# Performance work log

Hardware: AMD Instinct MI355X
Metric: run time of the kernel (lower is better)

## Reference

```python
import jax, jax.numpy as jnp
import numpy as np

B, D, K = 32768, 256, 2048
BETA = 0.25


def setup_inputs() -> dict:
    key = jax.random.key(0)
    k1, k2 = jax.random.split(key)
    latents = jax.random.normal(k1, (B, D), dtype=jnp.float32)
    # nn.Embedding weight initialized uniform(-1/K, 1/K)
    embedding = jax.random.uniform(k2, (K, D), dtype=jnp.float32,
                                   minval=-1.0 / K, maxval=1.0 / K)
    return {"latents": latents, "embedding": embedding}


def reference(latents, embedding):
    # Squared-L2 distances: [B, K]
    dist = (jnp.sum(latents ** 2, axis=1, keepdims=True)
            + jnp.sum(embedding ** 2, axis=1)
            - 2.0 * jnp.matmul(latents, embedding.T))
    encoding_inds = jnp.argmin(dist, axis=1)  # [B]

    # Gather codebook rows (equivalent to one-hot @ embedding)
    quantized = embedding[encoding_inds]  # [B, D]

    commitment_loss = jnp.mean((jax.lax.stop_gradient(quantized) - latents) ** 2)
    embedding_loss = jnp.mean((quantized - jax.lax.stop_gradient(latents)) ** 2)
    vq_loss = commitment_loss * BETA + embedding_loss

    # Straight-through estimator
    quantized_st = latents + jax.lax.stop_gradient(quantized - latents)

    # avg_probs = mean of one-hot over batch == normalized histogram of inds
    counts = jnp.zeros((K,), dtype=jnp.float32).at[encoding_inds].add(1.0)
    avg_probs = counts / B
    entropy_vq = -jnp.sum(avg_probs * jnp.log(avg_probs + 1e-10))

    # dist values at selected codes
    cluster_metric = jnp.mean(
        jnp.take_along_axis(dist, encoding_inds[:, None], axis=1))

    return (quantized_st, vq_loss, entropy_vq,
            encoding_inds[:, None], cluster_metric)
```

## Files before the change

### kernel.cpp

```cpp
#include <hip/hip_runtime.h>
#include <math.h>

#define B_ROWS 32768
#define D_DIM  256
#define K_CODES 2048

#define OUT_Q   0
#define OUT_VQ  8388608
#define OUT_ENT 8388609
#define OUT_IND 8388610
#define OUT_CM  8421378


#define WS_SE2   0
#define WS_SX2   8192
#define WS_CNT   139264
#define WS_PACK  147456
#define WS_MSEP  409600
#define WS_DISTP 475136
#define WS_BCAT  540672

typedef _Float16 f16x8 __attribute__((ext_vector_type(8)));
typedef float f32x4 __attribute__((ext_vector_type(4)));
typedef union { _Float16 h[4]; uint2 u2; } h4pack;

__global__ __launch_bounds__(256) void k_init(
    const float* __restrict__ X, const float* __restrict__ E,
    _Float16* __restrict__ A, _Float16* __restrict__ Bc,
    float* __restrict__ sx2, float* __restrict__ se2,
    unsigned long long* __restrict__ packed, int* __restrict__ counts) {
  int w = threadIdx.x >> 6, lane = threadIdx.x & 63;
  if (blockIdx.x < 8192) {
    int row = blockIdx.x * 4 + w;
    float4 v = ((const float4*)(X + (size_t)row * D_DIM))[lane];
    float s = v.x * v.x + v.y * v.y + v.z * v.z + v.w * v.w;
#pragma unroll
    for (int off = 32; off > 0; off >>= 1) s += __shfl_xor(s, off, 64);
    if (lane == 0) { sx2[row] = s; packed[row] = ~0ull; }
    h4pack hi, lo;
    hi.h[0] = (_Float16)v.x; hi.h[1] = (_Float16)v.y;
    hi.h[2] = (_Float16)v.z; hi.h[3] = (_Float16)v.w;
    lo.h[0] = (_Float16)((v.x - (float)hi.h[0]) * 4096.0f);
    lo.h[1] = (_Float16)((v.y - (float)hi.h[1]) * 4096.0f);
    lo.h[2] = (_Float16)((v.z - (float)hi.h[2]) * 4096.0f);
    lo.h[3] = (_Float16)((v.w - (float)hi.h[3]) * 4096.0f);
    *(uint2*)&A[(size_t)row * 512 + 4 * lane] = hi.u2;
    *(uint2*)&A[(size_t)row * 512 + 256 + 4 * lane] = lo.u2;
  } else {
    int bb = blockIdx.x - 8192;
    int row = bb * 4 + w;
    if (threadIdx.x < 4) counts[bb * 4 + threadIdx.x] = 0;
    float4 v = ((const float4*)(E + (size_t)row * D_DIM))[lane];
    float s = v.x * v.x + v.y * v.y + v.z * v.z + v.w * v.w;
#pragma unroll
    for (int off = 32; off > 0; off >>= 1) s += __shfl_xor(s, off, 64);
    if (lane == 0) se2[row] = s;
    const float S = 4194304.0f;
    const float SH = 0.000244140625f;
    float e0 = v.x * S, e1 = v.y * S, e2 = v.z * S, e3 = v.w * S;
    h4pack b1, b2, b3;
    b1.h[0] = (_Float16)e0; b1.h[1] = (_Float16)e1;
    b1.h[2] = (_Float16)e2; b1.h[3] = (_Float16)e3;
    b2.h[0] = (_Float16)((float)b1.h[0] * SH);
    b2.h[1] = (_Float16)((float)b1.h[1] * SH);
    b2.h[2] = (_Float16)((float)b1.h[2] * SH);
    b2.h[3] = (_Float16)((float)b1.h[3] * SH);
    b3.h[0] = (_Float16)(e0 - (float)b1.h[0]);
    b3.h[1] = (_Float16)(e1 - (float)b1.h[1]);
    b3.h[2] = (_Float16)(e2 - (float)b1.h[2]);
    b3.h[3] = (_Float16)(e3 - (float)b1.h[3]);
    *(uint2*)&Bc[(size_t)row * 768 + 4 * lane] = b1.u2;
    *(uint2*)&Bc[(size_t)row * 768 + 256 + 4 * lane] = b2.u2;
    *(uint2*)&Bc[(size_t)row * 768 + 512 + 4 * lane] = b3.u2;
  }
}

#define BARX() asm volatile("s_barrier" ::: "memory")

#define MFMA_QUAD(I0, J0)                                                    \
  do {                                                                       \
    __builtin_amdgcn_s_setprio(1);                                           \
    _Pragma("unroll") for (int ii = 0; ii < 4; ++ii) {                       \
      _Pragma("unroll") for (int jj = 0; jj < 2; ++jj) {                     \
        _Pragma("unroll") for (int kk = 0; kk < 2; ++kk) {                   \
          acc[(I0) + ii][(J0) + jj] =                                        \
              __builtin_amdgcn_mfma_f32_16x16x32_f16(                        \
                  af[ii * 2 + kk], bf[jj * 2 + kk],                          \
                  acc[(I0) + ii][(J0) + jj], 0, 0, 0);                       \
        }                                                                    \
      }                                                                      \
    }                                                                        \
    __builtin_amdgcn_s_setprio(0);                                           \
  } while (0)

__global__ __launch_bounds__(512, 2) void k_mfma2(
    const _Float16* __restrict__ A, const _Float16* __restrict__ Bc,
    const float* __restrict__ se2, const float* __restrict__ sx2,
    unsigned long long* __restrict__ packed) {
  extern __shared__ char smem[];
  const int tid = threadIdx.x;
  const int w = tid >> 6, lane = tid & 63;
  const int wm = w >> 2, wn = w & 3;
  const int q = lane >> 4, c = lane & 15;
  const int rowb = blockIdx.x & 127, colb = blockIdx.x >> 7;
  const int rowpan = rowb * 256, colpan = colb * 256;
  const int rsel = lane >> 3;
  const int chunkb = ((lane & 7) ^ rsel) * 16;
  const int rswz = c & 7;

  const char* Abase = (const char*)A;
  const char* Bbase = (const char*)Bc;
  char* sA = smem;
  char* sB = smem + 65536;

  auto issue = [&](int tt, int g, int bsel) {
    const int hh = (g == 3 || g == 4 || g == 5 || g == 7) ? 1 : 0;
    const int ss = (g == 2 || g == 4 || g == 6 || g == 7) ? 1 : 0;
    const int rl = hh * 128 + ss * 64 + w * 8 + rsel;
    const char* src;
    char* dst;
    if (g == 0 || g >= 5) {
      int aoff = (tt & 3) * 128 + (((tt >> 2) == 1) ? 512 : 0);
      src = Abase + ((size_t)(rowpan + rl) << 10) + aoff + chunkb;
      dst = sA + bsel * 32768 + hh * 16384 + ss * 8192 + w * 1024;
    } else {
      src = Bbase + (size_t)(colpan + rl) * 1536 + tt * 128 + chunkb;
      dst = sB + bsel * 32768 + hh * 16384 + ss * 8192 + w * 1024;
    }
    __builtin_amdgcn_global_load_lds(
        (const __attribute__((address_space(1))) unsigned int*)src,
        (__attribute__((address_space(3))) unsigned int*)dst, 16, 0, 0);
  };

  f32x4 acc[8][4];
#pragma unroll
  for (int i = 0; i < 8; ++i)
#pragma unroll
    for (int j = 0; j < 4; ++j) acc[i][j] = (f32x4){0.f, 0.f, 0.f, 0.f};

  auto lda = [&](f16x8* af, int ihalf, int bsel) {
#pragma unroll
    for (int ii = 0; ii < 4; ++ii)
#pragma unroll
      for (int kk = 0; kk < 2; ++kk) {
        int row = wm * 128 + (ihalf * 4 + ii) * 16 + c;
        int sl = ((kk * 4 + q) ^ rswz) * 16;
        af[ii * 2 + kk] = *(const f16x8*)(sA + bsel * 32768 + row * 128 + sl);
      }
  };
  auto ldb = [&](f16x8* bf, int j0, int bsel) {
#pragma unroll
    for (int jj = 0; jj < 2; ++jj)
#pragma unroll
      for (int kk = 0; kk < 2; ++kk) {
        int col = wn * 64 + (j0 + jj) * 16 + c;
        int sl = ((kk * 4 + q) ^ rswz) * 16;
        bf[jj * 2 + kk] = *(const f16x8*)(sB + bsel * 32768 + col * 128 + sl);
      }
  };

#pragma unroll
  for (int g = 0; g < 8; ++g) issue(0, g, 0);
  asm volatile("s_waitcnt vmcnt(2)" ::: "memory");
  BARX();

  f16x8 af[8], bf[4];

  for (int t = 0; t < 12; ++t) {
    const int bsel = t & 1;
    const int nb = bsel ^ 1;
    const bool pre = (t < 11);
    lda(af, 0, bsel);
    ldb(bf, 0, bsel);
    if (pre) { issue(t + 1, 0, nb); issue(t + 1, 1, nb); }
    BARX();
    MFMA_QUAD(0, 0);
    BARX();
    ldb(bf, 2, bsel);
    if (pre) { issue(t + 1, 2, nb); issue(t + 1, 3, nb); }
    BARX();
    MFMA_QUAD(0, 2);
    if (pre) asm volatile("s_waitcnt vmcnt(4)" ::: "memory");
    else     asm volatile("s_waitcnt vmcnt(0)" ::: "memory");
    BARX();
    lda(af, 1, bsel);
    if (pre) { issue(t + 1, 4, nb); issue(t + 1, 5, nb); }
    BARX();
    MFMA_QUAD(4, 2);
    BARX();
    ldb(bf, 0, bsel);
    if (pre) { issue(t + 1, 6, nb); issue(t + 1, 7, nb); }
    BARX();
    MFMA_QUAD(4, 0);
    if (pre) asm volatile("s_waitcnt vmcnt(2)" ::: "memory");
    BARX();
  }

  const float inv = 4.76837158203125e-07f;
  float se_j[4];
#pragma unroll
  for (int j = 0; j < 4; ++j) se_j[j] = se2[colpan + wn * 64 + j * 16 + c];
  unsigned long long* m = (unsigned long long*)smem;
#pragma unroll
  for (int i = 0; i < 8; ++i) {
    float4 sx4 = *(const float4*)&sx2[rowpan + wm * 128 + i * 16 + q * 4];
#pragma unroll
    for (int r = 0; r < 4; ++r) {
      float sx = ((const float*)&sx4)[r];
      float bs = 3.402823466e38f;
      int bk = 0;
#pragma unroll
      for (int j = 0; j < 4; ++j) {
        float t1 = sx + se_j[j];
        float d = t1 - acc[i][j][r] * inv;
        if (d < bs) { bs = d; bk = colpan + wn * 64 + j * 16 + c; }
      }
#pragma unroll
      for (int off = 1; off < 16; off <<= 1) {
        float os = __shfl_xor(bs, off, 64);
        int ok = __shfl_xor(bk, off, 64);
        if (os < bs || (os == bs && ok < bk)) { bs = os; bk = ok; }
      }
      if (c == 0) {
        m[wn * 256 + wm * 128 + i * 16 + q * 4 + r] =
            ((unsigned long long)__float_as_uint(bs) << 32) |
            (unsigned long long)(unsigned int)bk;
      }
    }
  }
  __syncthreads();
  if (tid < 256) {
    unsigned long long v = m[tid];
#pragma unroll
    for (int mm = 1; mm < 4; ++mm) {
      unsigned long long o = m[mm * 256 + tid];
      if (o < v) v = o;
    }
    atomicMin(&packed[rowpan + tid], v);
  }
}

__global__ __launch_bounds__(256) void k_gather(
    const float* __restrict__ X, const float* __restrict__ E,
    const unsigned long long* __restrict__ packed, float* __restrict__ outq,
    float* __restrict__ out_ind, int* __restrict__ counts,
    double* __restrict__ msep, double* __restrict__ distp) {
  __shared__ int sk[16];
  __shared__ float sd[16];
  int tid = threadIdx.x;
  if (tid < 16) {
    int row = blockIdx.x * 16 + tid;
    unsigned long long v = packed[row];
    int k = (int)(v & 0xFFFFFFFFull);
    sk[tid] = k;
    sd[tid] = __uint_as_float((unsigned int)(v >> 32));
    out_ind[row] = (float)k;
    atomicAdd(&counts[k], 1);
  }
  __syncthreads();
  int wave = tid >> 6, lane = tid & 63;
  double msum = 0.0, dsum = 0.0;
#pragma unroll
  for (int rr = 0; rr < 4; rr++) {
    int li = wave * 4 + rr;
    int b = blockIdx.x * 16 + li;
    int ind = sk[li];
    float4 x4 = ((const float4*)(X + (size_t)b * D_DIM))[lane];
    float4 q4 = ((const float4*)(E + (size_t)ind * D_DIM))[lane];
    float d0 = q4.x - x4.x, d1 = q4.y - x4.y, d2 = q4.z - x4.z, d3 = q4.w - x4.w;
    float4 o;
    o.x = x4.x + d0; o.y = x4.y + d1; o.z = x4.z + d2; o.w = x4.w + d3;
    ((float4*)(outq + (size_t)b * D_DIM))[lane] = o;
    float v = d0 * d0 + d1 * d1 + d2 * d2 + d3 * d3;
#pragma unroll
    for (int off = 32; off > 0; off >>= 1) v += __shfl_xor(v, off, 64);
    if (lane == 0) { msum += (double)v; dsum += (double)sd[li]; }
  }
  if (lane == 0) {
    int wg = blockIdx.x * 4 + wave;
    msep[wg] = msum;
    distp[wg] = dsum;
  }
}

__global__ __launch_bounds__(256) void k_final(
    const int* __restrict__ counts, const double* __restrict__ msep,
    const double* __restrict__ distp, float* __restrict__ out) {
  __shared__ double red[256];
  int t = threadIdx.x;

  double m = 0.0;
  for (int i = t; i < 8192; i += 256) m += msep[i];
  red[t] = m;
  __syncthreads();
  for (int s = 128; s > 0; s >>= 1) {
    if (t < s) red[t] += red[t + s];
    __syncthreads();
  }
  if (t == 0) {
    double mse = red[0] / ((double)B_ROWS * (double)D_DIM);
    out[OUT_VQ] = (float)(mse * 1.25);
  }
  __syncthreads();

  double d = 0.0;
  for (int i = t; i < 8192; i += 256) d += distp[i];
  red[t] = d;
  __syncthreads();
  for (int s = 128; s > 0; s >>= 1) {
    if (t < s) red[t] += red[t + s];
    __syncthreads();
  }
  if (t == 0) out[OUT_CM] = (float)(red[0] / (double)B_ROWS);
  __syncthreads();

  double e = 0.0;
  for (int k = t; k < K_CODES; k += 256) {
    float p = (float)counts[k] * (1.0f / 32768.0f);
    e += (double)(p * logf(p + 1e-10f));
  }
  red[t] = e;
  __syncthreads();
  for (int s = 128; s > 0; s >>= 1) {
    if (t < s) red[t] += red[t + s];
    __syncthreads();
  }
  if (t == 0) out[OUT_ENT] = (float)(-red[0]);
}

extern "C" void kernel_launch(void* const* d_in, const int* in_sizes, int n_in,
                              void* d_out, int out_size, void* d_ws,
                              size_t ws_size, hipStream_t stream) {
  const float* X = (const float*)d_in[0];
  const float* E = (const float*)d_in[1];
  float* out = (float*)d_out;
  char* ws = (char*)d_ws;
  float* se2 = (float*)(ws + WS_SE2);
  float* sx2 = (float*)(ws + WS_SX2);
  int* counts = (int*)(ws + WS_CNT);
  unsigned long long* packed = (unsigned long long*)(ws + WS_PACK);
  double* msep = (double*)(ws + WS_MSEP);
  double* distp = (double*)(ws + WS_DISTP);
  _Float16* Bcat = (_Float16*)(ws + WS_BCAT);
  _Float16* Acat = (_Float16*)d_out;

  static bool attr_done = false;
  if (!attr_done) {
    hipFuncSetAttribute((const void*)k_mfma2,
                        hipFuncAttributeMaxDynamicSharedMemorySize, 131072);
    attr_done = true;
  }

  k_init<<<8704, 256, 0, stream>>>(X, E, Acat, Bcat, sx2, se2, packed, counts);
  k_mfma2<<<1024, 512, 131072, stream>>>(Acat, Bcat, se2, sx2, packed);
  k_gather<<<B_ROWS / 16, 256, 0, stream>>>(X, E, packed, out + OUT_Q,
                                            out + OUT_IND, counts, msep, distp);
  k_final<<<1, 256, 0, stream>>>(counts, msep, distp, out);
}
```

Measured before the change: 262.5 us.

## Hand-schedule LDS reads with inline ds_read and double B fragment registers

Replaces compiler-generated LDS fragment loads with inline ds_read_b128 using immediate offsets. B fragments for both column halves are now held in separate register sets (bf01, bf23), which removes one reload and one barrier phase per k-step. Explicit lgkmcnt waits and sched_barriers pin the instruction order so loads are issued before barriers and MFMAs run after them. This trades higher VGPR pressure, which risks the 2-waves-per-SIMD occupancy target, and more rigid scheduling for fewer LDS reads and barriers.

```diff
diff --git a/kernel.cpp b/kernel.cpp
--- a/kernel.cpp
+++ b/kernel.cpp
@@ -75,9 +75,17 @@
   }
 }
 
-#define BARX() asm volatile("s_barrier" ::: "memory")
-
-#define MFMA_QUAD(I0, J0)                                                    \
+#define BAR()  __builtin_amdgcn_s_barrier()
+#define SB0()  __builtin_amdgcn_sched_barrier(0)
+#define WLGKM0()                                                \
+  do {                                                          \
+    asm volatile("s_waitcnt lgkmcnt(0)" ::: "memory");          \
+    SB0();                                                      \
+  } while (0)
+#define DSR(dst, a, o) \
+  asm volatile("ds_read_b128 %0, %1 offset:" o : "=v"(dst) : "v"(a))
+
+#define MFMA_QUAD(I0, J0, BF)                                                \
   do {                                                                       \
     __builtin_amdgcn_s_setprio(1);                                           \
     _Pragma("unroll") for (int ii = 0; ii < 4; ++ii) {                       \
@@ -85,7 +93,7 @@
         _Pragma("unroll") for (int kk = 0; kk < 2; ++kk) {                   \
           acc[(I0) + ii][(J0) + jj] =                                        \
               __builtin_amdgcn_mfma_f32_16x16x32_f16(                        \
-                  af[ii * 2 + kk], bf[jj * 2 + kk],                          \
+                  af[ii * 2 + kk], (BF)[jj * 2 + kk],                        \
                   acc[(I0) + ii][(J0) + jj], 0, 0, 0);                       \
         }                                                                    \
       }                                                                      \
@@ -110,8 +118,6 @@
 
   const char* Abase = (const char*)A;
   const char* Bbase = (const char*)Bc;
-  char* sA = smem;
-  char* sB = smem + 65536;
 
   auto issue = [&](int tt, int g, int bsel) {
     const int hh = (g == 3 || g == 4 || g == 5 || g == 7) ? 1 : 0;
@@ -122,10 +128,10 @@
     if (g == 0 || g >= 5) {
       int aoff = (tt & 3) * 128 + (((tt >> 2) == 1) ? 512 : 0);
       src = Abase + ((size_t)(rowpan + rl) << 10) + aoff + chunkb;
-      dst = sA + bsel * 32768 + hh * 16384 + ss * 8192 + w * 1024;
+      dst = smem + bsel * 32768 + hh * 16384 + ss * 8192 + w * 1024;
     } else {
       src = Bbase + (size_t)(colpan + rl) * 1536 + tt * 128 + chunkb;
-      dst = sB + bsel * 32768 + hh * 16384 + ss * 8192 + w * 1024;
+      dst = smem + 65536 + bsel * 32768 + hh * 16384 + ss * 8192 + w * 1024;
     }
     __builtin_amdgcn_global_load_lds(
         (const __attribute__((address_space(1))) unsigned int*)src,
@@ -138,63 +144,69 @@
 #pragma unroll
     for (int j = 0; j < 4; ++j) acc[i][j] = (f32x4){0.f, 0.f, 0.f, 0.f};
 
-  auto lda = [&](f16x8* af, int ihalf, int bsel) {
-#pragma unroll
-    for (int ii = 0; ii < 4; ++ii)
-#pragma unroll
-      for (int kk = 0; kk < 2; ++kk) {
-        int row = wm * 128 + (ihalf * 4 + ii) * 16 + c;
-        int sl = ((kk * 4 + q) ^ rswz) * 16;
-        af[ii * 2 + kk] = *(const f16x8*)(sA + bsel * 32768 + row * 128 + sl);
-      }
-  };
-  auto ldb = [&](f16x8* bf, int j0, int bsel) {
-#pragma unroll
-    for (int jj = 0; jj < 2; ++jj)
-#pragma unroll
-      for (int kk = 0; kk < 2; ++kk) {
-        int col = wn * 64 + (j0 + jj) * 16 + c;
-        int sl = ((kk * 4 + q) ^ rswz) * 16;
-        bf[jj * 2 + kk] = *(const f16x8*)(sB + bsel * 32768 + col * 128 + sl);
-      }
-  };
+  const unsigned ldsA = (unsigned)(uintptr_t)smem + (unsigned)((wm * 128 + c) * 128);
+  const unsigned ldsB = (unsigned)(uintptr_t)smem + 65536u +
+                        (unsigned)((wn * 64 + c) * 128);
+  const unsigned sl0 = (unsigned)(((0 * 4 + q) ^ rswz) * 16);
+  const unsigned sl1 = (unsigned)(((1 * 4 + q) ^ rswz) * 16);
 
 #pragma unroll
   for (int g = 0; g < 8; ++g) issue(0, g, 0);
   asm volatile("s_waitcnt vmcnt(2)" ::: "memory");
-  BARX();
-
-  f16x8 af[8], bf[4];
+  BAR();
+
+  f16x8 af[8], bf01[4], bf23[4];
 
   for (int t = 0; t < 12; ++t) {
     const int bsel = t & 1;
     const int nb = bsel ^ 1;
     const bool pre = (t < 11);
-    lda(af, 0, bsel);
-    ldb(bf, 0, bsel);
+    const unsigned aA0 = ldsA + (unsigned)(bsel * 32768) + sl0;
+    const unsigned aA1 = ldsA + (unsigned)(bsel * 32768) + sl1;
+    const unsigned aB0 = ldsB + (unsigned)(bsel * 32768) + sl0;
+    const unsigned aB1 = ldsB + (unsigned)(bsel * 32768) + sl1;
+
     if (pre) { issue(t + 1, 0, nb); issue(t + 1, 1, nb); }
-    BARX();
-    MFMA_QUAD(0, 0);
-    BARX();
-    ldb(bf, 2, bsel);
+    DSR(af[0], aA0, "0");    DSR(af[1], aA1, "0");
+    DSR(af[2], aA0, "2048"); DSR(af[3], aA1, "2048");
+    DSR(af[4], aA0, "4096"); DSR(af[5], aA1, "4096");
+    DSR(af[6], aA0, "6144"); DSR(af[7], aA1, "6144");
+    DSR(bf01[0], aB0, "0");    DSR(bf01[1], aB1, "0");
+    DSR(bf01[2], aB0, "2048"); DSR(bf01[3], aB1, "2048");
+    BAR();
+    WLGKM0();
+    MFMA_QUAD(0, 0, bf01);
+    SB0();
+    BAR();
+
     if (pre) { issue(t + 1, 2, nb); issue(t + 1, 3, nb); }
-    BARX();
-    MFMA_QUAD(0, 2);
+    DSR(bf23[0], aB0, "4096"); DSR(bf23[1], aB1, "4096");
+    DSR(bf23[2], aB0, "6144"); DSR(bf23[3], aB1, "6144");
+    BAR();
+    WLGKM0();
+    MFMA_QUAD(0, 2, bf23);
+    SB0();
     if (pre) asm volatile("s_waitcnt vmcnt(4)" ::: "memory");
     else     asm volatile("s_waitcnt vmcnt(0)" ::: "memory");
-    BARX();
-    lda(af, 1, bsel);
+    BAR();
+
     if (pre) { issue(t + 1, 4, nb); issue(t + 1, 5, nb); }
-    BARX();
-    MFMA_QUAD(4, 2);
-    BARX();
-    ldb(bf, 0, bsel);
+    DSR(af[0], aA0, "8192");  DSR(af[1], aA1, "8192");
+    DSR(af[2], aA0, "10240"); DSR(af[3], aA1, "10240");
+    DSR(af[4], aA0, "12288"); DSR(af[5], aA1, "12288");
+    DSR(af[6], aA0, "14336"); DSR(af[7], aA1, "14336");
+    BAR();
+    WLGKM0();
+    MFMA_QUAD(4, 2, bf23);
+    SB0();
     if (pre) { issue(t + 1, 6, nb); issue(t + 1, 7, nb); }
-    BARX();
-    MFMA_QUAD(4, 0);
+    MFMA_QUAD(4, 0, bf01);
+    SB0();
     if (pre) asm volatile("s_waitcnt vmcnt(2)" ::: "memory");
-    BARX();
-  }
+    BAR();
+  }
+
+  __syncthreads();
 
   const float inv = 4.76837158203125e-07f;
   float se_j[4];
```

Result: no change. 258.7 us (-1.5%).
